# Performance work log

Measured on AMD Instinct MI355X. Metric: run time of the kernel, lower is better.

Reference implementation:

```python
import jax, jax.numpy as jnp
import numpy as np

NUM_HEADS = 16
DIMS = 1024
B, P, C = 8, 1024, 1024
HEAD_DIMS = DIMS // NUM_HEADS


def setup_inputs() -> dict:
    key = jax.random.key(0)
    ks = jax.random.split(key, 10)
    s = 1.0 / np.sqrt(C)
    return {
        "q": jax.random.normal(ks[0], (B, P, C), jnp.float32),
        "x": jax.random.normal(ks[1], (B, P, C), jnp.float32),
        "Wq": jax.random.normal(ks[2], (C, DIMS), jnp.float32) * s,
        "bq": jnp.zeros((DIMS,), jnp.float32),
        "Wk": jax.random.normal(ks[3], (C, DIMS), jnp.float32) * s,
        "bk": jnp.zeros((DIMS,), jnp.float32),
        "Wv": jax.random.normal(ks[4], (C, DIMS), jnp.float32) * s,
        "bv": jnp.zeros((DIMS,), jnp.float32),
        "Wp": jax.random.normal(ks[5], (DIMS, DIMS), jnp.float32) * (1.0 / np.sqrt(DIMS)),
        "bp": jnp.zeros((DIMS,), jnp.float32),
    }


def reference(q, x, Wq, bq, Wk, bk, Wv, bv, Wp, bp):
    b, p, _ = x.shape
    hd, H = HEAD_DIMS, NUM_HEADS
    # Note: original reshapes Dense output to (B, P, head_dims, num_heads),
    # i.e. head index is the LAST axis -> head i gets strided feature columns.
    Q = (q @ Wq + bq).reshape(b, p, hd, H)  # [b, p, d, h]
    K = (x @ Wk + bk).reshape(b, p, hd, H)
    V = (x @ Wv + bv).reshape(b, p, hd, H)
    scores = jnp.einsum("bqdh,bkdh->bhqk", Q, K) / jnp.sqrt(jnp.asarray(hd, Q.dtype))
    weights = jax.nn.softmax(scores, axis=-1)  # dropout is identity (ratio 0)
    heads = jnp.einsum("bhqk,bkdh->bqhd", weights, V)  # [b, p, h, d]
    # Concatenate(axis=-1) of per-head outputs == head-major flatten of (h, d)
    out = heads.reshape(b, p, H * hd)
    return out @ Wp + bp
```

## Files before the change

kernel.cpp:

```cpp
#include <hip/hip_runtime.h>
#include <hip/hip_bf16.h>
#include <math.h>

#define NB   8
#define SEQ  1024
#define DIMS 1024
#define NH   16
#define HD   64
#define MROWS (NB*SEQ)

typedef unsigned short u16;
typedef short short8 __attribute__((ext_vector_type(8)));
typedef short short4v __attribute__((ext_vector_type(4)));
typedef float f32x4 __attribute__((ext_vector_type(4)));
typedef float f32x16 __attribute__((ext_vector_type(16)));

extern "C" __device__ float __ocml_native_exp2_f32(float);

__device__ inline u16 f2bf(float f) {
    unsigned u = __float_as_uint(f);
    u += 0x7fff + ((u >> 16) & 1);
    return (u16)(u >> 16);
}

__device__ inline unsigned pkbf(float a, float b) {
    float2 f2; f2.x = a; f2.y = b;
    __hip_bfloat162 h = __float22bfloat162_rn(f2);
    return *reinterpret_cast<unsigned*>(&h);
}

#define MFMA16(a, b, c) __builtin_amdgcn_mfma_f32_16x16x32_bf16((a), (b), (c), 0, 0, 0)
#define MFMA32(a, b, c) __builtin_amdgcn_mfma_f32_32x32x16_bf16((a), (b), (c), 0, 0, 0)
#define GLD16(g, l) __builtin_amdgcn_global_load_lds( \
    (const __attribute__((address_space(1))) void*)(g), \
    (__attribute__((address_space(3))) void*)(l), 16, 0, 0)

__global__ __launch_bounds__(256)
void convert_both(const float* __restrict__ qin, const float* __restrict__ xin,
                  u16* __restrict__ qo, u16* __restrict__ xo)
{
    const int half = (MROWS * DIMS / 8) / 256;
    const float* in = (blockIdx.x < half) ? qin : xin;
    u16* out        = (blockIdx.x < half) ? qo  : xo;
    int i = (blockIdx.x < half ? blockIdx.x : blockIdx.x - half) * 256 + threadIdx.x;
    float4 v0 = ((const float4*)in)[2 * i];
    float4 v1 = ((const float4*)in)[2 * i + 1];
    union { short8 s; u16 u[8]; } r;
    r.u[0] = f2bf(v0.x); r.u[1] = f2bf(v0.y); r.u[2] = f2bf(v0.z); r.u[3] = f2bf(v0.w);
    r.u[4] = f2bf(v1.x); r.u[5] = f2bf(v1.y); r.u[6] = f2bf(v1.z); r.u[7] = f2bf(v1.w);
    ((short8*)out)[i] = r.s;
}

__global__ __launch_bounds__(256)
void transpose_all(const float* __restrict__ W0, const float* __restrict__ W1,
                   const float* __restrict__ W2, const float* __restrict__ W3,
                   u16* __restrict__ T0, u16* __restrict__ T1o,
                   u16* __restrict__ T2, u16* __restrict__ T3)
{
    __shared__ u16 T[64][72];
    const int which = blockIdx.x >> 8;
    const int idx   = blockIdx.x & 255;
    const float* W = which == 0 ? W0 : which == 1 ? W1 : which == 2 ? W2 : W3;
    u16*        Wt = which == 0 ? T0 : which == 1 ? T1o : which == 2 ? T2 : T3;
    const int t  = threadIdx.x;
    const int k0 = (idx >> 4) * 64;
    const int n0 = (idx & 15) * 64;
    #pragma unroll
    for (int it = 0; it < 4; ++it) {
        int f  = t + it * 256;
        int kl = f >> 4;
        int n4 = (f & 15) * 4;
        float4 v = *(const float4*)&W[(size_t)(k0 + kl) * DIMS + n0 + n4];
        T[n4 + 0][kl] = f2bf(v.x);
        T[n4 + 1][kl] = f2bf(v.y);
        T[n4 + 2][kl] = f2bf(v.z);
        T[n4 + 3][kl] = f2bf(v.w);
    }
    __syncthreads();
    #pragma unroll
    for (int it = 0; it < 2; ++it) {
        int c  = t + it * 256;
        int nl = c >> 3;
        int k8 = (c & 7) * 8;
        *(short8*)&Wt[(size_t)(n0 + nl) * DIMS + k0 + k8] = *(const short8*)&T[nl][k8];
    }
}

__global__ __launch_bounds__(256)
void gemm_qkv(const u16* __restrict__ qb, const u16* __restrict__ xb,
              const u16* __restrict__ Wqt, const u16* __restrict__ Wkt,
              const u16* __restrict__ Wvt,
              const float* __restrict__ bq, const float* __restrict__ bk,
              const float* __restrict__ bv,
              u16* __restrict__ Qm, u16* __restrict__ Km, u16* __restrict__ Vm,
              float qscale)
{
    __shared__ u16 sm[17408];
    u16* As = sm;
    u16* Bs = sm + 8192;

    const int t    = threadIdx.x;
    const int w    = t >> 6, lane = t & 63;
    const int lo   = lane & 15, hi = lane >> 4;
    const int wg   = blockIdx.x;
    const int swzb = (wg & 7) * 192 + (wg >> 3);
    const int which = swzb / 512;
    const int rem   = swzb - which * 512;
    const int bn   = rem & 7;
    const int bm   = rem >> 3;
    const int m0   = bm * 128, n0 = bn * 128;
    const int wm   = (w >> 1) * 64, wn = (w & 1) * 64;

    const u16* A    = which == 0 ? qb  : xb;
    const u16* Bt   = which == 0 ? Wqt : which == 1 ? Wkt : Wvt;
    const float* bias = which == 0 ? bq : which == 1 ? bk : bv;
    const float scale = which == 0 ? qscale : 1.0f;

    f32x4 acc[4][4];
    #pragma unroll
    for (int mf = 0; mf < 4; ++mf)
        #pragma unroll
        for (int nf = 0; nf < 4; ++nf) acc[mf][nf] = (f32x4){0.f, 0.f, 0.f, 0.f};

    const u16* ga[4]; const u16* gb[4]; u16* la[4]; u16* lb[4];
    #pragma unroll
    for (int i = 0; i < 4; ++i) {
        int c   = (w * 4 + i) * 64 + lane;
        int row = c >> 3, kc = c & 7;
        ga[i] = A  + (size_t)(m0 + row) * 1024 + kc * 8;
        gb[i] = Bt + (size_t)(n0 + row) * 1024 + kc * 8;
        la[i] = As + (w * 4 + i) * 512;
        lb[i] = Bs + (w * 4 + i) * 512;
    }

    for (int kt = 0; kt < 16; ++kt) {
        if (kt) __syncthreads();
        #pragma unroll
        for (int i = 0; i < 4; ++i) {
            GLD16(ga[i] + kt * 64, la[i]);
            GLD16(gb[i] + kt * 64, lb[i]);
        }
        __syncthreads();

        #pragma unroll
        for (int s = 0; s < 2; ++s) {
            short8 fa[4], fb[4];
            #pragma unroll
            for (int mf = 0; mf < 4; ++mf)
                fa[mf] = *(const short8*)&As[(wm + mf * 16 + lo) * 64 + s * 32 + hi * 8];
            #pragma unroll
            for (int nf = 0; nf < 4; ++nf)
                fb[nf] = *(const short8*)&Bs[(wn + nf * 16 + lo) * 64 + s * 32 + hi * 8];
            #pragma unroll
            for (int mf = 0; mf < 4; ++mf)
                #pragma unroll
                for (int nf = 0; nf < 4; ++nf)
                    acc[mf][nf] = MFMA16(fa[mf], fb[nf], acc[mf][nf]);
        }
    }

    __syncthreads();
    if (which < 2) {
        u16* out = which == 0 ? Qm : Km;
        #pragma unroll
        for (int mf = 0; mf < 4; ++mf)
            #pragma unroll
            for (int j = 0; j < 4; ++j) {
                int pl = wm + mf * 16 + hi * 4 + j;
                #pragma unroll
                for (int nf = 0; nf < 4; ++nf) {
                    int nl = wn + nf * 16 + lo;
                    int h = nl & 15, dl = nl >> 4;
                    float v = (acc[mf][nf][j] + bias[n0 + nl]) * scale;
                    sm[pl * 136 + h * 8 + dl] = f2bf(v);
                }
            }
        __syncthreads();
        const int bb = m0 >> 10, p0 = m0 & 1023, dg = n0 >> 4;
        #pragma unroll
        for (int it = 0; it < 8; ++it) {
            int c = t + it * 256;
            int h = c & 15, pl = c >> 4;
            u16* dst = out + ((size_t)((bb * NH + h) * SEQ + p0 + pl)) * HD + dg;
            *(short8*)dst = *(const short8*)&sm[pl * 136 + h * 8];
        }
    } else {
        #pragma unroll
        for (int mf = 0; mf < 4; ++mf)
            #pragma unroll
            for (int j = 0; j < 4; ++j) {
                int pl = wm + mf * 16 + hi * 4 + j;
                #pragma unroll
                for (int nf = 0; nf < 4; ++nf) {
                    int nl = wn + nf * 16 + lo;
                    sm[nl * 136 + pl] = f2bf(acc[mf][nf][j] + bias[n0 + nl]);
                }
            }
        __syncthreads();
        const int bb = m0 >> 10, p0 = m0 & 1023;
        #pragma unroll
        for (int it = 0; it < 8; ++it) {
            int c  = t + it * 256;
            int nl = c >> 4, p8 = c & 15;
            int ng = n0 + nl;
            int h = ng & 15, d = ng >> 4;
            u16* dstrow = Vm + ((size_t)((bb * NH + h) * HD + d)) * SEQ + p0;
            const u16* src = &sm[nl * 136 + p8 * 8];
            int base16 = (p8 >> 1) * 16, c8 = p8 & 1;
            *(short4v*)&dstrow[base16 + c8 * 4]     = *(const short4v*)&src[0];
            *(short4v*)&dstrow[base16 + c8 * 4 + 8] = *(const short4v*)&src[4];
        }
    }
}

__global__ __launch_bounds__(256)
void gemm_out(const u16* __restrict__ A, const u16* __restrict__ Bt,
              const float* __restrict__ bias, float* __restrict__ out)
{
    __shared__ u16 sm[16384];
    u16* As = sm;
    u16* Bs = sm + 8192;

    const int t    = threadIdx.x;
    const int w    = t >> 6, lane = t & 63;
    const int lo   = lane & 15, hi = lane >> 4;
    const int wg   = blockIdx.x;
    const int swzb = (wg & 7) * 64 + (wg >> 3);
    const int bn   = swzb & 7;
    const int bm   = swzb >> 3;
    const int m0   = bm * 128, n0 = bn * 128;
    const int wm   = (w >> 1) * 64, wn = (w & 1) * 64;

    f32x4 acc[4][4];
    #pragma unroll
    for (int mf = 0; mf < 4; ++mf)
        #pragma unroll
        for (int nf = 0; nf < 4; ++nf) acc[mf][nf] = (f32x4){0.f, 0.f, 0.f, 0.f};

    const u16* ga[4]; const u16* gb[4]; u16* la[4]; u16* lb[4];
    #pragma unroll
    for (int i = 0; i < 4; ++i) {
        int c   = (w * 4 + i) * 64 + lane;
        int row = c >> 3, kc = c & 7;
        ga[i] = A  + (size_t)(m0 + row) * 1024 + kc * 8;
        gb[i] = Bt + (size_t)(n0 + row) * 1024 + kc * 8;
        la[i] = As + (w * 4 + i) * 512;
        lb[i] = Bs + (w * 4 + i) * 512;
    }

    for (int kt = 0; kt < 16; ++kt) {
        if (kt) __syncthreads();
        #pragma unroll
        for (int i = 0; i < 4; ++i) {
            GLD16(ga[i] + kt * 64, la[i]);
            GLD16(gb[i] + kt * 64, lb[i]);
        }
        __syncthreads();

        #pragma unroll
        for (int s = 0; s < 2; ++s) {
            short8 fa[4], fb[4];
            #pragma unroll
            for (int mf = 0; mf < 4; ++mf)
                fa[mf] = *(const short8*)&As[(wm + mf * 16 + lo) * 64 + s * 32 + hi * 8];
            #pragma unroll
            for (int nf = 0; nf < 4; ++nf)
                fb[nf] = *(const short8*)&Bs[(wn + nf * 16 + lo) * 64 + s * 32 + hi * 8];
            #pragma unroll
            for (int mf = 0; mf < 4; ++mf)
                #pragma unroll
                for (int nf = 0; nf < 4; ++nf)
                    acc[mf][nf] = MFMA16(fa[mf], fb[nf], acc[mf][nf]);
        }
    }

    #pragma unroll
    for (int mf = 0; mf < 4; ++mf)
        #pragma unroll
        for (int j = 0; j < 4; ++j) {
            int r = m0 + wm + mf * 16 + hi * 4 + j;
            #pragma unroll
            for (int nf = 0; nf < 4; ++nf) {
                int cc = n0 + wn + nf * 16 + lo;
                out[(size_t)r * 1024 + cc] = acc[mf][nf][j] + bias[cc];
            }
        }
}

__global__ __launch_bounds__(512, 4)
void attn_mfma32_kernel(const u16* __restrict__ Qm, const u16* __restrict__ Km,
                        const u16* __restrict__ Vp, u16* __restrict__ heads)
{
    __shared__ u16 KV[2][8192];

    const int t  = threadIdx.x;
    const int w  = t >> 6, lane = t & 63;
    const int ql = lane & 31, h5 = lane >> 5;

    const int wg  = blockIdx.x;
    const int swz = (wg & 7) * 64 + (wg >> 3);
    const int qb  = swz & 3;
    const int bh  = swz >> 2;
    const int q0  = qb * 256 + w * 32;
    const size_t kbase = (size_t)bh * (SEQ * HD);
    const size_t vbase = (size_t)bh * (HD * SEQ);

    const int lc = t ^ ((t >> 3) & 7);
    const u16* gK = Km + kbase + (size_t)lc * 8;
    const u16* gV = Vp + vbase + (size_t)(t >> 3) * SEQ + (lc & 7) * 8;
    const int ldK = w * 512;
    const int ldV = 4096 + w * 512;

#define STAGE(B, T) do { \
    GLD16(gK + (size_t)(T) * 4096, &KV[B][ldK]); \
    GLD16(gV + (T) * 64,           &KV[B][ldV]); } while (0)

    STAGE(0, 0);

    short8 qf[4];
    #pragma unroll
    for (int td = 0; td < 4; ++td)
        qf[td] = *(const short8*)&Qm[kbase + (size_t)(q0 + ql) * HD + td * 16 + h5 * 8];

    const int sw0 = (ql & 7) << 3;
    const int rb0 = ql * 64, rb1 = (32 + ql) * 64;
    int kof[4];
    #pragma unroll
    for (int i = 0; i < 4; ++i)
        kof[i] = (i * 16 + h5 * 8) ^ sw0;

    f32x16 o0, o1;
    #pragma unroll
    for (int i = 0; i < 16; ++i) { o0[i] = 0.f; o1[i] = 0.f; }
    float ls0 = 0.f, ls1 = 0.f, ls2 = 0.f, ls3 = 0.f;

    __syncthreads();

    for (int tile = 0; tile < 16; ++tile) {
        const int buf = tile & 1;
        if (tile < 15) STAGE(buf ^ 1, tile + 1);

        const u16* Kb = &KV[buf][0];
        const u16* Vb = &KV[buf][4096];

        f32x16 sc0, sc1;
        #pragma unroll
        for (int i = 0; i < 16; ++i) { sc0[i] = 0.f; sc1[i] = 0.f; }
        {
            short8 k0 = *(const short8*)&Kb[rb0 + kof[0]];
            short8 k1 = *(const short8*)&Kb[rb0 + kof[1]];
            short8 k2 = *(const short8*)&Kb[rb0 + kof[2]];
            short8 k3 = *(const short8*)&Kb[rb0 + kof[3]];
            sc0 = MFMA32(k0, qf[0], sc0);
            sc0 = MFMA32(k1, qf[1], sc0);
            sc0 = MFMA32(k2, qf[2], sc0);
            sc0 = MFMA32(k3, qf[3], sc0);
            short8 m0_ = *(const short8*)&Kb[rb1 + kof[0]];
            short8 m1_ = *(const short8*)&Kb[rb1 + kof[1]];
            short8 m2_ = *(const short8*)&Kb[rb1 + kof[2]];
            short8 m3_ = *(const short8*)&Kb[rb1 + kof[3]];
            sc1 = MFMA32(m0_, qf[0], sc1);
            sc1 = MFMA32(m1_, qf[1], sc1);
            sc1 = MFMA32(m2_, qf[2], sc1);
            sc1 = MFMA32(m3_, qf[3], sc1);
        }

        #pragma unroll
        for (int i = 0; i < 16; i += 4) {
            float p0 = __ocml_native_exp2_f32(sc0[i + 0]);
            float p1 = __ocml_native_exp2_f32(sc0[i + 1]);
            float p2 = __ocml_native_exp2_f32(sc0[i + 2]);
            float p3 = __ocml_native_exp2_f32(sc0[i + 3]);
            sc0[i + 0] = p0; sc0[i + 1] = p1; sc0[i + 2] = p2; sc0[i + 3] = p3;
            ls0 += p0; ls1 += p1; ls2 += p2; ls3 += p3;
        }
        #pragma unroll
        for (int i = 0; i < 16; i += 4) {
            float p0 = __ocml_native_exp2_f32(sc1[i + 0]);
            float p1 = __ocml_native_exp2_f32(sc1[i + 1]);
            float p2 = __ocml_native_exp2_f32(sc1[i + 2]);
            float p3 = __ocml_native_exp2_f32(sc1[i + 3]);
            sc1[i + 0] = p0; sc1[i + 1] = p1; sc1[i + 2] = p2; sc1[i + 3] = p3;
            ls0 += p0; ls1 += p1; ls2 += p2; ls3 += p3;
        }

#define PVSTEP(S, TAU, B8) { \
        union { unsigned u[4]; short8 sv; } pb; \
        pb.u[0] = pkbf(S[B8 + 0], S[B8 + 1]); \
        pb.u[1] = pkbf(S[B8 + 2], S[B8 + 3]); \
        pb.u[2] = pkbf(S[B8 + 4], S[B8 + 5]); \
        pb.u[3] = pkbf(S[B8 + 6], S[B8 + 7]); \
        const int vcs = (((TAU) * 16 + h5 * 8) ^ sw0); \
        short8 vf0 = *(const short8*)&Vb[rb0 + vcs]; \
        short8 vf1 = *(const short8*)&Vb[rb1 + vcs]; \
        o0 = MFMA32(vf0, pb.sv, o0); \
        o1 = MFMA32(vf1, pb.sv, o1); }

        PVSTEP(sc0, 0, 0);
        PVSTEP(sc0, 1, 8);
        PVSTEP(sc1, 2, 0);
        PVSTEP(sc1, 3, 8);
#undef PVSTEP

        if (tile < 15) __syncthreads();
    }

    float l_run = (ls0 + ls1) + (ls2 + ls3);
    float l_tot = l_run + __shfl_xor(l_run, 32);
    float inv = 1.0f / l_tot;

    __syncthreads();
    u16* Ot = &KV[0][0];
    const int bb = bh >> 4, hh = bh & 15;
    const int obase = w * 1280;

    #pragma unroll
    for (int pass = 0; pass < 2; ++pass) {
        #pragma unroll
        for (int r = 0; r < 16; r += 2) {
            int dl = (r & 3) + 8 * (r >> 2) + 4 * h5;
            float a = (pass ? o1[r]     : o0[r])     * inv;
            float b = (pass ? o1[r + 1] : o0[r + 1]) * inv;
            *(unsigned*)&Ot[obase + ql * 40 + dl] = pkbf(a, b);
        }
        __syncthreads();
        #pragma unroll
        for (int i = 0; i < 2; ++i) {
            int dl = h5 * 16 + i * 8;
            short8 vv = *(const short8*)&Ot[obase + ql * 40 + dl];
            int d = pass * 32 + dl;
            *(short8*)&heads[((size_t)(bb * SEQ + q0 + ql) * NH + hh) * HD + d] = vv;
        }
        __syncthreads();
    }
#undef STAGE
}

extern "C" void kernel_launch(void* const* d_in, const int* in_sizes, int n_in,
                              void* d_out, int out_size, void* d_ws, size_t ws_size,
                              hipStream_t stream) {
    const float* q  = (const float*)d_in[0];
    const float* x  = (const float*)d_in[1];
    const float* Wq = (const float*)d_in[2];
    const float* bq = (const float*)d_in[3];
    const float* Wk = (const float*)d_in[4];
    const float* bk = (const float*)d_in[5];
    const float* Wv = (const float*)d_in[6];
    const float* bv = (const float*)d_in[7];
    const float* Wp = (const float*)d_in[8];
    const float* bp = (const float*)d_in[9];
    float* out = (float*)d_out;

    const size_t SZ = (size_t)MROWS * DIMS;
    const size_t WZ = (size_t)DIMS * DIMS;
    u16* qb  = (u16*)d_ws;
    u16* xb  = qb  + SZ;
    u16* Wqt = xb  + SZ;
    u16* Wkt = Wqt + WZ;
    u16* Wvt = Wkt + WZ;
    u16* Wpt = Wvt + WZ;
    u16* Qm  = Wpt + WZ;
    u16* Km  = Qm  + SZ;
    u16* Vm  = Km  + SZ;
    u16* Hm  = Vm  + SZ;

    const float qscale = 0.125f * 1.4426950408889634f;

    hipLaunchKernelGGL(convert_both, dim3(8192), dim3(256), 0, stream, q, x, qb, xb);
    hipLaunchKernelGGL(transpose_all, dim3(1024), dim3(256), 0, stream,
                       Wq, Wk, Wv, Wp, Wqt, Wkt, Wvt, Wpt);
    hipLaunchKernelGGL(gemm_qkv, dim3(1536), dim3(256), 0, stream,
                       qb, xb, Wqt, Wkt, Wvt, bq, bk, bv, Qm, Km, Vm, qscale);
    hipLaunchKernelGGL(attn_mfma32_kernel, dim3(512), dim3(512), 0, stream, Qm, Km, Vm, Hm);
    hipLaunchKernelGGL(gemm_out, dim3(512), dim3(256), 0, stream, Hm, Wpt, bp, out);
}
```

Baseline: 182.8 us.

## Double-buffer LDS tiles in QKV and output GEMMs with K-step of 32

```diff
diff --git a/kernel.cpp b/kernel.cpp
--- a/kernel.cpp
+++ b/kernel.cpp
@@ -96,8 +96,8 @@
               float qscale)
 {
     __shared__ u16 sm[17408];
-    u16* As = sm;
-    u16* Bs = sm + 8192;
+    u16* buf0 = sm;
+    u16* buf1 = sm + 8192;
 
     const int t    = threadIdx.x;
     const int w    = t >> 6, lane = t & 63;
@@ -111,8 +111,8 @@
     const int m0   = bm * 128, n0 = bn * 128;
     const int wm   = (w >> 1) * 64, wn = (w & 1) * 64;
 
-    const u16* A    = which == 0 ? qb  : xb;
-    const u16* Bt   = which == 0 ? Wqt : which == 1 ? Wkt : Wvt;
+    const u16* A      = which == 0 ? qb  : xb;
+    const u16* Bt     = which == 0 ? Wqt : which == 1 ? Wkt : Wvt;
     const float* bias = which == 0 ? bq : which == 1 ? bk : bv;
     const float scale = which == 0 ? qscale : 1.0f;
 
@@ -122,44 +122,50 @@
         #pragma unroll
         for (int nf = 0; nf < 4; ++nf) acc[mf][nf] = (f32x4){0.f, 0.f, 0.f, 0.f};
 
-    const u16* ga[4]; const u16* gb[4]; u16* la[4]; u16* lb[4];
-    #pragma unroll
-    for (int i = 0; i < 4; ++i) {
-        int c   = (w * 4 + i) * 64 + lane;
-        int row = c >> 3, kc = c & 7;
+    const u16* ga[2]; const u16* gb[2]; int laOff[2], lbOff[2];
+    #pragma unroll
+    for (int i = 0; i < 2; ++i) {
+        int c   = i * 256 + t;
+        int row = c >> 2, kc = c & 3;
         ga[i] = A  + (size_t)(m0 + row) * 1024 + kc * 8;
         gb[i] = Bt + (size_t)(n0 + row) * 1024 + kc * 8;
-        la[i] = As + (w * 4 + i) * 512;
-        lb[i] = Bs + (w * 4 + i) * 512;
-    }
-
-    for (int kt = 0; kt < 16; ++kt) {
-        if (kt) __syncthreads();
-        #pragma unroll
-        for (int i = 0; i < 4; ++i) {
-            GLD16(ga[i] + kt * 64, la[i]);
-            GLD16(gb[i] + kt * 64, lb[i]);
-        }
-        __syncthreads();
-
-        #pragma unroll
-        for (int s = 0; s < 2; ++s) {
-            short8 fa[4], fb[4];
-            #pragma unroll
-            for (int mf = 0; mf < 4; ++mf)
-                fa[mf] = *(const short8*)&As[(wm + mf * 16 + lo) * 64 + s * 32 + hi * 8];
-            #pragma unroll
-            for (int nf = 0; nf < 4; ++nf)
-                fb[nf] = *(const short8*)&Bs[(wn + nf * 16 + lo) * 64 + s * 32 + hi * 8];
-            #pragma unroll
-            for (int mf = 0; mf < 4; ++mf)
-                #pragma unroll
-                for (int nf = 0; nf < 4; ++nf)
-                    acc[mf][nf] = MFMA16(fa[mf], fb[nf], acc[mf][nf]);
-        }
-    }
-
+        laOff[i] = (i * 256 + w * 64) * 8;
+        lbOff[i] = 4096 + (i * 256 + w * 64) * 8;
+    }
+
+#define STAGE(BUF, KT) do { \
+    GLD16(ga[0] + (KT) * 32, (BUF) + laOff[0]); \
+    GLD16(ga[1] + (KT) * 32, (BUF) + laOff[1]); \
+    GLD16(gb[0] + (KT) * 32, (BUF) + lbOff[0]); \
+    GLD16(gb[1] + (KT) * 32, (BUF) + lbOff[1]); } while (0)
+
+#define COMPUTE(BUF) do { \
+    short8 fa[4], fb[4]; \
+    _Pragma("unroll") \
+    for (int mf = 0; mf < 4; ++mf) \
+        fa[mf] = *(const short8*)&(BUF)[(wm + mf * 16 + lo) * 32 + hi * 8]; \
+    _Pragma("unroll") \
+    for (int nf = 0; nf < 4; ++nf) \
+        fb[nf] = *(const short8*)&(BUF)[4096 + (wn + nf * 16 + lo) * 32 + hi * 8]; \
+    _Pragma("unroll") \
+    for (int mf = 0; mf < 4; ++mf) \
+        _Pragma("unroll") \
+        for (int nf = 0; nf < 4; ++nf) \
+            acc[mf][nf] = MFMA16(fa[mf], fb[nf], acc[mf][nf]); } while (0)
+
+    STAGE(buf0, 0);
     __syncthreads();
+    for (int kt = 0; kt < 32; kt += 2) {
+        STAGE(buf1, kt + 1);
+        COMPUTE(buf0);
+        __syncthreads();
+        if (kt + 2 < 32) STAGE(buf0, kt + 2);
+        COMPUTE(buf1);
+        __syncthreads();
+    }
+#undef STAGE
+#undef COMPUTE
+
     if (which < 2) {
         u16* out = which == 0 ? Qm : Km;
         #pragma unroll
@@ -218,8 +224,8 @@
               const float* __restrict__ bias, float* __restrict__ out)
 {
     __shared__ u16 sm[16384];
-    u16* As = sm;
-    u16* Bs = sm + 8192;
+    u16* buf0 = sm;
+    u16* buf1 = sm + 8192;
 
     const int t    = threadIdx.x;
     const int w    = t >> 6, lane = t & 63;
@@ -237,42 +243,49 @@
         #pragma unroll
         for (int nf = 0; nf < 4; ++nf) acc[mf][nf] = (f32x4){0.f, 0.f, 0.f, 0.f};
 
-    const u16* ga[4]; const u16* gb[4]; u16* la[4]; u16* lb[4];
-    #pragma unroll
-    for (int i = 0; i < 4; ++i) {
-        int c   = (w * 4 + i) * 64 + lane;
-        int row = c >> 3, kc = c & 7;
+    const u16* ga[2]; const u16* gb[2]; int laOff[2], lbOff[2];
+    #pragma unroll
+    for (int i = 0; i < 2; ++i) {
+        int c   = i * 256 + t;
+        int row = c >> 2, kc = c & 3;
         ga[i] = A  + (size_t)(m0 + row) * 1024 + kc * 8;
         gb[i] = Bt + (size_t)(n0 + row) * 1024 + kc * 8;
-        la[i] = As + (w * 4 + i) * 512;
-        lb[i] = Bs + (w * 4 + i) * 512;
-    }
-
-    for (int kt = 0; kt < 16; ++kt) {
-        if (kt) __syncthreads();
-        #pragma unroll
-        for (int i = 0; i < 4; ++i) {
-            GLD16(ga[i] + kt * 64, la[i]);
-            GLD16(gb[i] + kt * 64, lb[i]);
-        }
-        __syncthreads();
-
-        #pragma unroll
-        for (int s = 0; s < 2; ++s) {
-            short8 fa[4], fb[4];
-            #pragma unroll
-            for (int mf = 0; mf < 4; ++mf)
-                fa[mf] = *(const short8*)&As[(wm + mf * 16 + lo) * 64 + s * 32 + hi * 8];
-            #pragma unroll
-            for (int nf = 0; nf < 4; ++nf)
-                fb[nf] = *(const short8*)&Bs[(wn + nf * 16 + lo) * 64 + s * 32 + hi * 8];
-            #pragma unroll
-            for (int mf = 0; mf < 4; ++mf)
-                #pragma unroll
-                for (int nf = 0; nf < 4; ++nf)
-                    acc[mf][nf] = MFMA16(fa[mf], fb[nf], acc[mf][nf]);
-        }
-    }
+        laOff[i] = (i * 256 + w * 64) * 8;
+        lbOff[i] = 4096 + (i * 256 + w * 64) * 8;
+    }
+
+#define STAGE(BUF, KT) do { \
+    GLD16(ga[0] + (KT) * 32, (BUF) + laOff[0]); \
+    GLD16(ga[1] + (KT) * 32, (BUF) + laOff[1]); \
+    GLD16(gb[0] + (KT) * 32, (BUF) + lbOff[0]); \
+    GLD16(gb[1] + (KT) * 32, (BUF) + lbOff[1]); } while (0)
+
+#define COMPUTE(BUF) do { \
+    short8 fa[4], fb[4]; \
+    _Pragma("unroll") \
+    for (int mf = 0; mf < 4; ++mf) \
+        fa[mf] = *(const short8*)&(BUF)[(wm + mf * 16 + lo) * 32 + hi * 8]; \
+    _Pragma("unroll") \
+    for (int nf = 0; nf < 4; ++nf) \
+        fb[nf] = *(const short8*)&(BUF)[4096 + (wn + nf * 16 + lo) * 32 + hi * 8]; \
+    _Pragma("unroll") \
+    for (int mf = 0; mf < 4; ++mf) \
+        _Pragma("unroll") \
+        for (int nf = 0; nf < 4; ++nf) \
+            acc[mf][nf] = MFMA16(fa[mf], fb[nf], acc[mf][nf]); } while (0)
+
+    STAGE(buf0, 0);
+    __syncthreads();
+    for (int kt = 0; kt < 32; kt += 2) {
+        STAGE(buf1, kt + 1);
+        COMPUTE(buf0);
+        __syncthreads();
+        if (kt + 2 < 32) STAGE(buf0, kt + 2);
+        COMPUTE(buf1);
+        __syncthreads();
+    }
+#undef STAGE
+#undef COMPUTE
 
     #pragma unroll
     for (int mf = 0; mf < 4; ++mf)
```

Result: faster. 171.6 us (-6.1%).

## Rewrite projection GEMMs with 256x128 tiles, triple-buffered LDS and swizzled layout

Applied to the files above, without the earlier changes.

```diff
diff --git a/kernel.cpp b/kernel.cpp
--- a/kernel.cpp
+++ b/kernel.cpp
@@ -86,126 +86,166 @@
     }
 }
 
-__global__ __launch_bounds__(256)
-void gemm_qkv(const u16* __restrict__ qb, const u16* __restrict__ xb,
-              const u16* __restrict__ Wqt, const u16* __restrict__ Wkt,
-              const u16* __restrict__ Wvt,
-              const float* __restrict__ bq, const float* __restrict__ bk,
-              const float* __restrict__ bv,
-              u16* __restrict__ Qm, u16* __restrict__ Km, u16* __restrict__ Vm,
-              float qscale)
+#define GEMM_CORE(A_, Bt_)                                                     \
+    const int lo = lane & 15, hi = lane >> 4;                                  \
+    const int wM = w >> 1, wN = w & 1;                                         \
+    const u16* gA[4]; const u16* gB[2];                                        \
+    _Pragma("unroll")                                                          \
+    for (int i = 0; i < 4; ++i) {                                              \
+        int c = i * 512 + t, row = c >> 3, kc = c & 7;                         \
+        gA[i] = A_ + (size_t)(m0 + row) * 1024 + (kc ^ (row & 7)) * 8;         \
+    }                                                                          \
+    _Pragma("unroll")                                                          \
+    for (int i = 0; i < 2; ++i) {                                              \
+        int c = i * 512 + t, row = c >> 3, kc = c & 7;                         \
+        gB[i] = Bt_ + (size_t)(n0 + row) * 1024 + (kc ^ (row & 7)) * 8;        \
+    }                                                                          \
+    int rowA[4], rowB[4];                                                      \
+    _Pragma("unroll")                                                          \
+    for (int mf = 0; mf < 4; ++mf) rowA[mf] = (wM * 64 + mf * 16 + lo) * 64;   \
+    _Pragma("unroll")                                                          \
+    for (int nf = 0; nf < 4; ++nf) rowB[nf] = 16384 + (wN * 64 + nf * 16 + lo) * 64; \
+    const int ko0 = (hi * 8) ^ ((lo & 7) << 3);                                \
+    const int ko1 = (32 + hi * 8) ^ ((lo & 7) << 3);                           \
+    f32x4 acc[4][4];                                                           \
+    _Pragma("unroll")                                                          \
+    for (int mf = 0; mf < 4; ++mf)                                             \
+        _Pragma("unroll")                                                      \
+        for (int nf = 0; nf < 4; ++nf) acc[mf][nf] = (f32x4){0.f,0.f,0.f,0.f}; \
+                                                \
+    _Pragma("unroll")                                                          \
+    for (int i = 0; i < 4; ++i) GLD16(gA[i],      smem + i * 4096 + w * 512);  \
+    _Pragma("unroll")                                                          \
+    for (int i = 0; i < 2; ++i) GLD16(gB[i],      smem + 16384 + i * 4096 + w * 512); \
+    _Pragma("unroll")                                                          \
+    for (int i = 0; i < 4; ++i) GLD16(gA[i] + 64, smem + 24576 + i * 4096 + w * 512); \
+    _Pragma("unroll")                                                          \
+    for (int i = 0; i < 2; ++i) GLD16(gB[i] + 64, smem + 24576 + 16384 + i * 4096 + w * 512); \
+    asm volatile("s_waitcnt vmcnt(6)" ::: "memory");                           \
+    __builtin_amdgcn_s_barrier();                                              \
+    int b0 = 0, b1 = 24576, b2 = 49152;                                        \
+    for (int kt = 0; kt < 16; ++kt) {                                          \
+                     \
+        if (kt < 14) {                                                         \
+            GLD16(gA[0] + (size_t)(kt + 2) * 64, smem + b2 + 0 * 4096 + w * 512);        \
+            GLD16(gA[1] + (size_t)(kt + 2) * 64, smem + b2 + 1 * 4096 + w * 512);        \
+            GLD16(gB[0] + (size_t)(kt + 2) * 64, smem + b2 + 16384 + 0 * 4096 + w * 512);\
+        }                                                                      \
+        {                                                                      \
+            short8 fa[4], fb[4];                                               \
+            _Pragma("unroll")                                                  \
+            for (int mf = 0; mf < 4; ++mf) fa[mf] = *(const short8*)&smem[b0 + rowA[mf] + ko0]; \
+            _Pragma("unroll")                                                  \
+            for (int nf = 0; nf < 4; ++nf) fb[nf] = *(const short8*)&smem[b0 + rowB[nf] + ko0]; \
+            __builtin_amdgcn_s_setprio(1);                                     \
+            _Pragma("unroll")                                                  \
+            for (int mf = 0; mf < 4; ++mf)                                     \
+                _Pragma("unroll")                                              \
+                for (int nf = 0; nf < 4; ++nf)                                 \
+                    acc[mf][nf] = MFMA16(fa[mf], fb[nf], acc[mf][nf]);         \
+            __builtin_amdgcn_s_setprio(0);                                     \
+        }                                                                      \
+        __builtin_amdgcn_s_barrier();                                          \
+                  \
+        if (kt < 14) {                                                         \
+            GLD16(gA[2] + (size_t)(kt + 2) * 64, smem + b2 + 2 * 4096 + w * 512);        \
+            GLD16(gA[3] + (size_t)(kt + 2) * 64, smem + b2 + 3 * 4096 + w * 512);        \
+            GLD16(gB[1] + (size_t)(kt + 2) * 64, smem + b2 + 16384 + 1 * 4096 + w * 512);\
+        }                                                                      \
+        {                                                                      \
+            short8 fa[4], fb[4];                                               \
+            _Pragma("unroll")                                                  \
+            for (int mf = 0; mf < 4; ++mf) fa[mf] = *(const short8*)&smem[b0 + rowA[mf] + ko1]; \
+            _Pragma("unroll")                                                  \
+            for (int nf = 0; nf < 4; ++nf) fb[nf] = *(const short8*)&smem[b0 + rowB[nf] + ko1]; \
+            __builtin_amdgcn_s_setprio(1);                                     \
+            _Pragma("unroll")                                                  \
+            for (int mf = 0; mf < 4; ++mf)                                     \
+                _Pragma("unroll")                                              \
+                for (int nf = 0; nf < 4; ++nf)                                 \
+                    acc[mf][nf] = MFMA16(fa[mf], fb[nf], acc[mf][nf]);         \
+            __builtin_amdgcn_s_setprio(0);                                     \
+        }                                                                      \
+        if (kt < 14) { asm volatile("s_waitcnt vmcnt(6)" ::: "memory"); }      \
+        else         { asm volatile("s_waitcnt vmcnt(0)" ::: "memory"); }      \
+        __builtin_amdgcn_s_barrier();                                          \
+        int tmp = b0; b0 = b1; b1 = b2; b2 = tmp;                              \
+    }
+
+__global__ __launch_bounds__(512, 2)
+void gemm_qkv8(const u16* __restrict__ qb, const u16* __restrict__ xb,
+               const u16* __restrict__ Wqt, const u16* __restrict__ Wkt,
+               const u16* __restrict__ Wvt,
+               const float* __restrict__ bq, const float* __restrict__ bk,
+               const float* __restrict__ bv,
+               u16* __restrict__ Qm, u16* __restrict__ Km, u16* __restrict__ Vm,
+               float qscale)
 {
-    __shared__ u16 sm[17408];
-    u16* As = sm;
-    u16* Bs = sm + 8192;
-
-    const int t    = threadIdx.x;
-    const int w    = t >> 6, lane = t & 63;
-    const int lo   = lane & 15, hi = lane >> 4;
+    extern __shared__ u16 smem[];
+    const int t = threadIdx.x;
+    const int w = t >> 6, lane = t & 63;
+
     const int wg   = blockIdx.x;
-    const int swzb = (wg & 7) * 192 + (wg >> 3);
-    const int which = swzb / 512;
-    const int rem   = swzb - which * 512;
-    const int bn   = rem & 7;
-    const int bm   = rem >> 3;
-    const int m0   = bm * 128, n0 = bn * 128;
-    const int wm   = (w >> 1) * 64, wn = (w & 1) * 64;
-
-    const u16* A    = which == 0 ? qb  : xb;
-    const u16* Bt   = which == 0 ? Wqt : which == 1 ? Wkt : Wvt;
+    const int swzb = (wg & 7) * 96 + (wg >> 3);
+    const int which = swzb >> 8;
+    const int rem   = swzb & 255;
+    const int bn = rem & 7, bm = rem >> 3;
+    const int m0 = bm * 256, n0 = bn * 128;
+
+    const u16* A      = which == 0 ? qb  : xb;
+    const u16* Bt     = which == 0 ? Wqt : which == 1 ? Wkt : Wvt;
     const float* bias = which == 0 ? bq : which == 1 ? bk : bv;
     const float scale = which == 0 ? qscale : 1.0f;
 
-    f32x4 acc[4][4];
-    #pragma unroll
-    for (int mf = 0; mf < 4; ++mf)
-        #pragma unroll
-        for (int nf = 0; nf < 4; ++nf) acc[mf][nf] = (f32x4){0.f, 0.f, 0.f, 0.f};
-
-    const u16* ga[4]; const u16* gb[4]; u16* la[4]; u16* lb[4];
-    #pragma unroll
-    for (int i = 0; i < 4; ++i) {
-        int c   = (w * 4 + i) * 64 + lane;
-        int row = c >> 3, kc = c & 7;
-        ga[i] = A  + (size_t)(m0 + row) * 1024 + kc * 8;
-        gb[i] = Bt + (size_t)(n0 + row) * 1024 + kc * 8;
-        la[i] = As + (w * 4 + i) * 512;
-        lb[i] = Bs + (w * 4 + i) * 512;
-    }
-
-    for (int kt = 0; kt < 16; ++kt) {
-        if (kt) __syncthreads();
-        #pragma unroll
-        for (int i = 0; i < 4; ++i) {
-            GLD16(ga[i] + kt * 64, la[i]);
-            GLD16(gb[i] + kt * 64, lb[i]);
-        }
-        __syncthreads();
-
-        #pragma unroll
-        for (int s = 0; s < 2; ++s) {
-            short8 fa[4], fb[4];
-            #pragma unroll
-            for (int mf = 0; mf < 4; ++mf)
-                fa[mf] = *(const short8*)&As[(wm + mf * 16 + lo) * 64 + s * 32 + hi * 8];
-            #pragma unroll
-            for (int nf = 0; nf < 4; ++nf)
-                fb[nf] = *(const short8*)&Bs[(wn + nf * 16 + lo) * 64 + s * 32 + hi * 8];
-            #pragma unroll
-            for (int mf = 0; mf < 4; ++mf)
-                #pragma unroll
-                for (int nf = 0; nf < 4; ++nf)
-                    acc[mf][nf] = MFMA16(fa[mf], fb[nf], acc[mf][nf]);
-        }
-    }
+    GEMM_CORE(A, Bt)
 
     __syncthreads();
+    const int bb = m0 >> 10, p0 = m0 & 1023;
     if (which < 2) {
         u16* out = which == 0 ? Qm : Km;
         #pragma unroll
         for (int mf = 0; mf < 4; ++mf)
             #pragma unroll
             for (int j = 0; j < 4; ++j) {
-                int pl = wm + mf * 16 + hi * 4 + j;
+                int pl = wM * 64 + mf * 16 + hi * 4 + j;
                 #pragma unroll
                 for (int nf = 0; nf < 4; ++nf) {
-                    int nl = wn + nf * 16 + lo;
+                    int nl = wN * 64 + nf * 16 + lo;
                     int h = nl & 15, dl = nl >> 4;
                     float v = (acc[mf][nf][j] + bias[n0 + nl]) * scale;
-                    sm[pl * 136 + h * 8 + dl] = f2bf(v);
+                    smem[pl * 136 + h * 8 + dl] = f2bf(v);
                 }
             }
         __syncthreads();
-        const int bb = m0 >> 10, p0 = m0 & 1023, dg = n0 >> 4;
+        const int dg = n0 >> 4;
         #pragma unroll
         for (int it = 0; it < 8; ++it) {
-            int c = t + it * 256;
+            int c = t + it * 512;
             int h = c & 15, pl = c >> 4;
             u16* dst = out + ((size_t)((bb * NH + h) * SEQ + p0 + pl)) * HD + dg;
-            *(short8*)dst = *(const short8*)&sm[pl * 136 + h * 8];
+            *(short8*)dst = *(const short8*)&smem[pl * 136 + h * 8];
         }
     } else {
         #pragma unroll
         for (int mf = 0; mf < 4; ++mf)
             #pragma unroll
             for (int j = 0; j < 4; ++j) {
-                int pl = wm + mf * 16 + hi * 4 + j;
+                int pl = wM * 64 + mf * 16 + hi * 4 + j;
                 #pragma unroll
                 for (int nf = 0; nf < 4; ++nf) {
-                    int nl = wn + nf * 16 + lo;
-                    sm[nl * 136 + pl] = f2bf(acc[mf][nf][j] + bias[n0 + nl]);
+                    int nl = wN * 64 + nf * 16 + lo;
+                    smem[nl * 264 + pl] = f2bf(acc[mf][nf][j] + bias[n0 + nl]);
                 }
             }
         __syncthreads();
-        const int bb = m0 >> 10, p0 = m0 & 1023;
         #pragma unroll
         for (int it = 0; it < 8; ++it) {
-            int c  = t + it * 256;
-            int nl = c >> 4, p8 = c & 15;
+            int c  = t + it * 512;
+            int nl = c >> 5, p8 = c & 31;
             int ng = n0 + nl;
             int h = ng & 15, d = ng >> 4;
             u16* dstrow = Vm + ((size_t)((bb * NH + h) * HD + d)) * SEQ + p0;
-            const u16* src = &sm[nl * 136 + p8 * 8];
+            const u16* src = &smem[nl * 264 + p8 * 8];
             int base16 = (p8 >> 1) * 16, c8 = p8 & 1;
             *(short4v*)&dstrow[base16 + c8 * 4]     = *(const short4v*)&src[0];
             *(short4v*)&dstrow[base16 + c8 * 4 + 8] = *(const short4v*)&src[4];
@@ -213,75 +253,29 @@
     }
 }
 
-__global__ __launch_bounds__(256)
-void gemm_out(const u16* __restrict__ A, const u16* __restrict__ Bt,
-              const float* __restrict__ bias, float* __restrict__ out)
+__global__ __launch_bounds__(512, 2)
+void gemm_out8(const u16* __restrict__ Am, const u16* __restrict__ Btm,
+               const float* __restrict__ bias, float* __restrict__ out)
 {
-    __shared__ u16 sm[16384];
-    u16* As = sm;
-    u16* Bs = sm + 8192;
-
-    const int t    = threadIdx.x;
-    const int w    = t >> 6, lane = t & 63;
-    const int lo   = lane & 15, hi = lane >> 4;
+    extern __shared__ u16 smem[];
+    const int t = threadIdx.x;
+    const int w = t >> 6, lane = t & 63;
+
     const int wg   = blockIdx.x;
-    const int swzb = (wg & 7) * 64 + (wg >> 3);
-    const int bn   = swzb & 7;
-    const int bm   = swzb >> 3;
-    const int m0   = bm * 128, n0 = bn * 128;
-    const int wm   = (w >> 1) * 64, wn = (w & 1) * 64;
-
-    f32x4 acc[4][4];
+    const int swzb = (wg & 7) * 32 + (wg >> 3);
+    const int bn = swzb & 7, bm = swzb >> 3;
+    const int m0 = bm * 256, n0 = bn * 128;
+
+    GEMM_CORE(Am, Btm)
+
     #pragma unroll
     for (int mf = 0; mf < 4; ++mf)
         #pragma unroll
-        for (int nf = 0; nf < 4; ++nf) acc[mf][nf] = (f32x4){0.f, 0.f, 0.f, 0.f};
-
-    const u16* ga[4]; const u16* gb[4]; u16* la[4]; u16* lb[4];
-    #pragma unroll
-    for (int i = 0; i < 4; ++i) {
-        int c   = (w * 4 + i) * 64 + lane;
-        int row = c >> 3, kc = c & 7;
-        ga[i] = A  + (size_t)(m0 + row) * 1024 + kc * 8;
-        gb[i] = Bt + (size_t)(n0 + row) * 1024 + kc * 8;
-        la[i] = As + (w * 4 + i) * 512;
-        lb[i] = Bs + (w * 4 + i) * 512;
-    }
-
-    for (int kt = 0; kt < 16; ++kt) {
-        if (kt) __syncthreads();
-        #pragma unroll
-        for (int i = 0; i < 4; ++i) {
-            GLD16(ga[i] + kt * 64, la[i]);
-            GLD16(gb[i] + kt * 64, lb[i]);
-        }
-        __syncthreads();
-
-        #pragma unroll
-        for (int s = 0; s < 2; ++s) {
-            short8 fa[4], fb[4];
-            #pragma unroll
-            for (int mf = 0; mf < 4; ++mf)
-                fa[mf] = *(const short8*)&As[(wm + mf * 16 + lo) * 64 + s * 32 + hi * 8];
-            #pragma unroll
-            for (int nf = 0; nf < 4; ++nf)
-                fb[nf] = *(const short8*)&Bs[(wn + nf * 16 + lo) * 64 + s * 32 + hi * 8];
-            #pragma unroll
-            for (int mf = 0; mf < 4; ++mf)
-                #pragma unroll
-                for (int nf = 0; nf < 4; ++nf)
-                    acc[mf][nf] = MFMA16(fa[mf], fb[nf], acc[mf][nf]);
-        }
-    }
-
-    #pragma unroll
-    for (int mf = 0; mf < 4; ++mf)
-        #pragma unroll
         for (int j = 0; j < 4; ++j) {
-            int r = m0 + wm + mf * 16 + hi * 4 + j;
+            int r = m0 + wM * 64 + mf * 16 + hi * 4 + j;
             #pragma unroll
             for (int nf = 0; nf < 4; ++nf) {
-                int cc = n0 + wn + nf * 16 + lo;
+                int cc = n0 + wN * 64 + nf * 16 + lo;
                 out[(size_t)r * 1024 + cc] = acc[mf][nf][j] + bias[cc];
             }
         }
@@ -465,12 +459,18 @@
     u16* Hm  = Vm  + SZ;
 
     const float qscale = 0.125f * 1.4426950408889634f;
+    const int LDS_BYTES = 147456;
+
+    hipFuncSetAttribute((const void*)gemm_qkv8,
+                        hipFuncAttributeMaxDynamicSharedMemorySize, LDS_BYTES);
+    hipFuncSetAttribute((const void*)gemm_out8,
+                        hipFuncAttributeMaxDynamicSharedMemorySize, LDS_BYTES);
 
     hipLaunchKernelGGL(convert_both, dim3(8192), dim3(256), 0, stream, q, x, qb, xb);
     hipLaunchKernelGGL(transpose_all, dim3(1024), dim3(256), 0, stream,
                        Wq, Wk, Wv, Wp, Wqt, Wkt, Wvt, Wpt);
-    hipLaunchKernelGGL(gemm_qkv, dim3(1536), dim3(256), 0, stream,
+    hipLaunchKernelGGL(gemm_qkv8, dim3(768), dim3(512), LDS_BYTES, stream,
                        qb, xb, Wqt, Wkt, Wvt, bq, bk, bv, Qm, Km, Vm, qscale);
     hipLaunchKernelGGL(attn_mfma32_kernel, dim3(512), dim3(512), 0, stream, Qm, Km, Vm, Hm);
-    hipLaunchKernelGGL(gemm_out, dim3(512), dim3(256), 0, stream, Hm, Wpt, bp, out);
-}
+    hipLaunchKernelGGL(gemm_out8, dim3(256), dim3(512), LDS_BYTES, stream, Hm, Wpt, bp, out);
+}
```

Result: faster. 158.8 us (-13.1%).
